# Performance work log

Hardware: AMD Instinct MI355X
Metric: run time of the kernel (lower is better)

Reference implementation:

```python
import jax, jax.numpy as jnp
import numpy as np

D = 512    # feature_dim
NH = 8     # n_head
LQ = 1024  # query length
LK = 1024  # key/value length
B = 4      # batch
TEMP = 30.0


def setup_inputs() -> dict:
    key = jax.random.key(0)
    ks = jax.random.split(key, 10)
    s = (2.0 / D) ** 0.5  # init: normal(0, sqrt(2/out_features))
    t = lambda k, shp: jax.random.normal(k, shp, dtype=jnp.float32)
    return {
        'query_real': t(ks[0], (LQ, B, D)),
        'query_imag': t(ks[1], (LQ, B, D)),
        'key_real': t(ks[2], (LK, B, D)),
        'key_imag': t(ks[3], (LK, B, D)),
        'value_real': t(ks[4], (LK, B, D)),
        'value_imag': t(ks[5], (LK, B, D)),
        # per-head stacked Linear weights [NH, out, in] (torch Linear: x @ W.T + b)
        'WK_real': t(ks[6], (NH, D, D)) * s,
        'WK_imag': t(ks[7], (NH, D, D)) * s,
        'WV_real': t(ks[8], (NH, D, D)) * s,
        'WV_imag': t(ks[9], (NH, D, D)) * s,
        'bK_real': jnp.zeros((NH, D), jnp.float32),
        'bK_imag': jnp.zeros((NH, D), jnp.float32),
        'bV_real': jnp.zeros((NH, D), jnp.float32),
        'bV_imag': jnp.zeros((NH, D), jnp.float32),
    }


def reference(query_real, query_imag, key_real, key_imag, value_real, value_imag,
              WK_real, WK_imag, WV_real, WV_imag,
              bK_real, bK_imag, bV_real, bV_imag):
    # stacked per-head linear: x [L,B,D], W [H,E,D], b [H,E] -> [H,L,B,E]
    lin = lambda x, W, b: jnp.einsum('lbd,hed->hlbe', x, W) + b[:, None, None, :]
    # complex projection of keys with WK (real/imag parts)
    kr = lin(key_real, WK_real, bK_real) - lin(key_imag, WK_imag, bK_imag)
    ki = lin(key_real, WK_imag, bK_imag) + lin(key_imag, WK_real, bK_real)
    # queries are projected with the WV weights (as in the source)
    qr = lin(query_real, WV_real, bV_real) - lin(query_imag, WV_imag, bV_imag)
    qi = lin(query_real, WV_imag, bV_imag) + lin(query_imag, WV_real, bV_real)
    # complex dot product q*k (no conjugate), magnitude -> scores [H,B,Lq,Lk]
    dr = jnp.einsum('hqbd,hpbd->hbqp', qr, kr) - jnp.einsum('hqbd,hpbd->hbqp', qi, ki)
    di = jnp.einsum('hqbd,hpbd->hbqp', qi, kr) + jnp.einsum('hqbd,hpbd->hbqp', qr, ki)
    mag = jnp.sqrt(dr * dr + di * di)
    aff = jax.nn.softmax(mag * TEMP, axis=-1)  # softmax over keys
    # weighted value sum; values are the RAW inputs (not projected)
    out_real = jnp.einsum('hbqp,pbd->qbhd', aff, value_real).reshape(LQ, B, NH * D)
    out_imag = jnp.einsum('hbqp,pbd->qbhd', aff, value_imag).reshape(LQ, B, NH * D)
    return out_real, out_imag
```

## Files before the change

kernel.cpp:

```cpp
#include <hip/hip_runtime.h>
#include <math.h>

typedef _Float16 h8_t __attribute__((ext_vector_type(8)));
typedef _Float16 h4_t __attribute__((ext_vector_type(4)));
typedef float    f4_t __attribute__((ext_vector_type(4)));

#define MFMA16(a, b, c) __builtin_amdgcn_mfma_f32_16x16x32_f16((a), (b), (c), 0, 0, 0)

typedef const __attribute__((address_space(1))) void* gas1_t;
typedef __attribute__((address_space(3))) void* las3_t;
__device__ __forceinline__ void gload16(const void* g, void* l) {
  __builtin_amdgcn_global_load_lds((gas1_t)g, (las3_t)l, 16, 0, 0);
}

constexpr int L   = 1024;
constexpr int NB  = 4;
constexpr int NHh = 8;
constexpr int D   = 512;
constexpr int M1  = L * NB;
constexpr int K1  = 2 * D;
constexpr int N1  = NHh * 2 * D;
constexpr int HB  = NHh * NB;

constexpr size_t PL_A2 = (size_t)HB * L * K1 * 2;
constexpr size_t PL_BS = (size_t)HB * 3 * L * D * 2;
constexpr size_t OFF_R0 = 0;
constexpr size_t OFF_A2 = 134217728;
constexpr size_t OFF_BS = OFF_A2 + 2 * PL_A2;
constexpr size_t OFF_VT = OFF_BS + 2 * PL_BS;
constexpr size_t WS_NEED = OFF_VT + (size_t)NB * 1024 * 1024 * 2;
constexpr size_t PL_AX = (size_t)M1 * K1 * 2;
constexpr size_t ST_AQ = 0;
constexpr size_t ST_AK = 2 * PL_AX;
constexpr size_t PL_W  = (size_t)N1 * K1 * 2;
constexpr size_t ST_WQ = 4 * PL_AX;
constexpr size_t ST_WK = ST_WQ + 2 * PL_W;

static __device__ __forceinline__ void split32(float x, _Float16& hi, _Float16& lo) {
  _Float16 h = (_Float16)x;
  hi = h;
  lo = (_Float16)(x - (float)h);
}


__global__ void k_stage_x(const float* __restrict__ qre, const float* __restrict__ qim,
                          const float* __restrict__ kre, const float* __restrict__ kim,
                          _Float16* __restrict__ qhi, _Float16* __restrict__ qlo,
                          _Float16* __restrict__ khi, _Float16* __restrict__ klo) {
  const float* re; const float* im; _Float16* hi; _Float16* lo;
  if (blockIdx.y == 0) { re = qre; im = qim; hi = qhi; lo = qlo; }
  else                 { re = kre; im = kim; hi = khi; lo = klo; }
  int t = blockIdx.x * 256 + threadIdx.x;
  size_t idx = (size_t)t * 4;
  int m = (int)(idx >> 10), k = (int)(idx & 1023);
  const float* src = (k < 512) ? (re + (size_t)m * 512 + k) : (im + (size_t)m * 512 + (k - 512));
  f4_t v = *reinterpret_cast<const f4_t*>(src);
  h4_t h, l;
#pragma unroll
  for (int j = 0; j < 4; ++j) {
    _Float16 hh, ll; split32(v[j], hh, ll); h[j] = hh; l[j] = ll;
  }
  int sw = ((m >> 1) & 3) << 3;
  size_t dst = (size_t)m * 1024 + (k ^ sw);
  *reinterpret_cast<h4_t*>(hi + dst) = h;
  *reinterpret_cast<h4_t*>(lo + dst) = l;
}

__global__ void k_stage_w(const float* __restrict__ WVr, const float* __restrict__ WVi,
                          const float* __restrict__ WKr, const float* __restrict__ WKi,
                          _Float16* __restrict__ qhi, _Float16* __restrict__ qlo,
                          _Float16* __restrict__ khi, _Float16* __restrict__ klo) {
  const float* Wr; const float* Wi; _Float16* hi; _Float16* lo;
  if (blockIdx.y == 0) { Wr = WVr; Wi = WVi; hi = qhi; lo = qlo; }
  else                 { Wr = WKr; Wi = WKi; hi = khi; lo = klo; }
  int t = blockIdx.x * 256 + threadIdx.x;
  size_t idx = (size_t)t * 4;
  int n = (int)(idx >> 10), k = (int)(idx & 1023);
  int h = n >> 10, ri = (n >> 9) & 1, e = n & 511;
  size_t rowoff = ((size_t)(h * 512 + e)) * 512;
  const float* src; float sgn = 1.0f;
  if (ri == 0) {
    if (k < 512) src = Wr + rowoff + k;
    else { src = Wi + rowoff + (k - 512); sgn = -1.0f; }
  } else {
    if (k < 512) src = Wi + rowoff + k;
    else src = Wr + rowoff + (k - 512);
  }
  f4_t v = *reinterpret_cast<const f4_t*>(src);
  h4_t h4, l4;
#pragma unroll
  for (int j = 0; j < 4; ++j) {
    _Float16 hh, ll; split32(sgn * v[j], hh, ll); h4[j] = hh; l4[j] = ll;
  }
  int sw = ((n >> 1) & 3) << 3;
  size_t dst = (size_t)n * 1024 + (k ^ sw);
  *reinterpret_cast<h4_t*>(hi + dst) = h4;
  *reinterpret_cast<h4_t*>(lo + dst) = l4;
}

__global__ void k_stage_v(const float* __restrict__ vr, const float* __restrict__ vi,
                          _Float16* __restrict__ vt) {
  __shared__ float tile[64][65];
  int pt = blockIdx.x, nt = blockIdx.y, b = blockIdx.z;
  const float* src = (nt < 8) ? vr : vi;
  int dbase = (nt & 7) * 64;
  for (int i = threadIdx.x; i < 4096; i += 256) {
    int pl = i >> 6, dl = i & 63;
    tile[pl][dl] = src[((size_t)(pt * 64 + pl) * 4 + b) * 512 + dbase + dl];
  }
  __syncthreads();
  for (int i = threadIdx.x; i < 4096; i += 256) {
    int nl = i >> 6, pl = i & 63;
    int psw = pl ^ ((nl & 7) << 3);
    vt[((size_t)b * 1024 + nt * 64 + nl) * 1024 + pt * 64 + psw] = (_Float16)tile[pl][nl];
  }
}

__global__ __launch_bounds__(512, 1) void k_proj(
    const _Float16* __restrict__ Ahi, const _Float16* __restrict__ Alo,
    const _Float16* __restrict__ Bhi, const _Float16* __restrict__ Blo,
    const float* __restrict__ biasR, const float* __restrict__ biasI,
    _Float16* __restrict__ OutHi, _Float16* __restrict__ OutLo, int mode) {
  extern __shared__ __align__(16) _Float16 dldsP[];
  const int tid = threadIdx.x;
  const int id = blockIdx.x;
  const int xcd = id & 7, j = id >> 3;
  const int cm = j >> 2, cn = j & 3;
  const int m0 = cm * 256;
  const int n0 = (xcd * 4 + cn) * 256;
  const int wid = tid >> 6, lane = tid & 63;
  const int wm = (wid >> 1) * 64, wn = (wid & 1) * 128;
  const int fr = lane & 15, fq = lane >> 4;
  const int csw = (fq ^ ((fr >> 1) & 3)) * 8;

  const int srow = tid >> 2, sslot = tid & 3;
  const int soff = srow * 32 + sslot * 8;
  const _Float16* gA0 = Ahi + (size_t)(m0 + srow) * 1024 + sslot * 8;
  const _Float16* gA1 = gA0 + 128 * 1024;
  const _Float16* gA2 = Alo + (size_t)(m0 + srow) * 1024 + sslot * 8;
  const _Float16* gA3 = gA2 + 128 * 1024;
  const _Float16* gB0 = Bhi + (size_t)(n0 + srow) * 1024 + sslot * 8;
  const _Float16* gB1 = gB0 + 128 * 1024;
  const _Float16* gB2 = Blo + (size_t)(n0 + srow) * 1024 + sslot * 8;
  const _Float16* gB3 = gB2 + 128 * 1024;

  auto STAGE = [&](int buf) {
    _Float16* Lb = dldsP + buf * 32768;
    gload16(gA0, &Lb[soff]);
    gload16(gA1, &Lb[4096 + soff]);
    gload16(gA2, &Lb[8192 + soff]);
    gload16(gA3, &Lb[12288 + soff]);
    gload16(gB0, &Lb[16384 + soff]);
    gload16(gB1, &Lb[20480 + soff]);
    gload16(gB2, &Lb[24576 + soff]);
    gload16(gB3, &Lb[28672 + soff]);
    gA0 += 32; gA1 += 32; gA2 += 32; gA3 += 32;
    gB0 += 32; gB1 += 32; gB2 += 32; gB3 += 32;
  };

  f4_t acc[4][8] = {};
  auto compute = [&](int buf) {
    const _Float16* Lb = dldsP + buf * 32768;
    h8_t af[4][2];
#pragma unroll
    for (int mi = 0; mi < 4; ++mi) {
      int r = wm + mi * 16 + fr;
      af[mi][0] = *reinterpret_cast<const h8_t*>(&Lb[r * 32 + csw]);
      af[mi][1] = *reinterpret_cast<const h8_t*>(&Lb[8192 + r * 32 + csw]);
    }
#pragma unroll
    for (int ni = 0; ni < 8; ++ni) {
      int rn = wn + ni * 16 + fr;
      h8_t bh = *reinterpret_cast<const h8_t*>(&Lb[16384 + rn * 32 + csw]);
      h8_t bl = *reinterpret_cast<const h8_t*>(&Lb[24576 + rn * 32 + csw]);
#pragma unroll
      for (int mi = 0; mi < 4; ++mi) {
        acc[mi][ni] = MFMA16(af[mi][0], bh, acc[mi][ni]);
        acc[mi][ni] = MFMA16(af[mi][0], bl, acc[mi][ni]);
        acc[mi][ni] = MFMA16(af[mi][1], bh, acc[mi][ni]);
      }
    }
  };

  STAGE(0);
  for (int kt = 0; kt < 31; ++kt) {
    __builtin_amdgcn_s_barrier();
    STAGE((kt + 1) & 1);
    asm volatile("s_waitcnt vmcnt(8)" ::: "memory");
    __builtin_amdgcn_s_barrier();
    compute(kt & 1);
  }
  __builtin_amdgcn_s_barrier();
  asm volatile("s_waitcnt vmcnt(0)" ::: "memory");
  __builtin_amdgcn_s_barrier();
  compute(1);

#pragma unroll
  for (int mi = 0; mi < 4; ++mi)
#pragma unroll
    for (int ni = 0; ni < 8; ++ni)
#pragma unroll
      for (int r = 0; r < 4; ++r) {
        int m = m0 + wm + mi * 16 + fq * 4 + r;
        int n = n0 + wn + ni * 16 + fr;
        int h = n >> 10, ri = (n >> 9) & 1, e = n & 511;
        float bias = (ri == 0) ? (biasR[h * 512 + e] - biasI[h * 512 + e])
                               : (biasI[h * 512 + e] + biasR[h * 512 + e]);
        float val = acc[mi][ni][r] + bias;
        _Float16 hi, lo; split32(val, hi, lo);
        int lb = m & 3;
        int lrow = m >> 2;
        int hb = h * 4 + lb;
        int sw = ((lrow >> 1) & 3) << 3;
        if (mode == 0) {
          size_t dst = ((size_t)hb * 1024 + lrow) * 1024 + ((ri * 512 + e) ^ sw);
          OutHi[dst] = hi; OutLo[dst] = lo;
        } else {
          int esw = e ^ sw;
          if (ri == 0) {
            size_t dst = (((size_t)hb * 3 + 0) * 1024 + lrow) * 512 + esw;
            OutHi[dst] = hi; OutLo[dst] = lo;
          } else {
            size_t d1 = (((size_t)hb * 3 + 1) * 1024 + lrow) * 512 + esw;
            size_t d2 = (((size_t)hb * 3 + 2) * 1024 + lrow) * 512 + esw;
            OutHi[d1] = hi;  OutLo[d1] = lo;
            OutHi[d2] = -hi; OutLo[d2] = -lo;
          }
        }
      }
}

__global__ __launch_bounds__(512, 1) void k_score(
    const _Float16* __restrict__ A2hi, const _Float16* __restrict__ A2lo,
    const _Float16* __restrict__ BShi, const _Float16* __restrict__ BSlo,
    float* __restrict__ mag) {
  extern __shared__ __align__(16) _Float16 dldsS[];
  const int tid = threadIdx.x;
  const int id = blockIdx.x;
  const int xcd = id & 7, j = id >> 3;
  const int hb = xcd * 4 + (j >> 5);
  const int r5 = j & 31;
  const int m0 = (r5 >> 3) * 256, n0 = (r5 & 7) * 128;
  const int wid = tid >> 6, lane = tid & 63;
  const int wm = (wid >> 1) * 64, wn = (wid & 1) * 64;
  const int fr = lane & 15, fq = lane >> 4;
  const int csw = (fq ^ ((fr >> 1) & 3)) * 8;

  const _Float16* Abh = A2hi + (size_t)hb * 1048576;
  const _Float16* Abl = A2lo + (size_t)hb * 1048576;
  const _Float16* BShb = BShi + (size_t)hb * 3 * 524288;
  const _Float16* BSlb = BSlo + (size_t)hb * 3 * 524288;

  const int srow = tid >> 2, sslot = tid & 3;
  const int soff = srow * 32 + sslot * 8;
  const size_t bbase = (size_t)(n0 + srow) * 512 + sslot * 8;
  const _Float16* gA0 = Abh + (size_t)(m0 + srow) * 1024 + sslot * 8;
  const _Float16* gA1 = gA0 + 128 * 1024;
  const _Float16* gA2 = Abl + (size_t)(m0 + srow) * 1024 + sslot * 8;
  const _Float16* gA3 = gA2 + 128 * 1024;
  const _Float16* gB0 = BShb + bbase;
  const _Float16* gB1 = BSlb + bbase;
  const _Float16* gB2 = BShb + 524288 + bbase;
  const _Float16* gB3 = BSlb + 524288 + bbase;

  auto STAGE = [&](int buf, int kt) {
    if (kt == 16) {
      gB0 = BShb + 2 * 524288 + bbase;
      gB1 = BSlb + 2 * 524288 + bbase;
      gB2 = BShb + bbase;
      gB3 = BSlb + bbase;
    }
    _Float16* Lb = dldsS + buf * 32768;
    gload16(gA0, &Lb[soff]);
    gload16(gA1, &Lb[4096 + soff]);
    gload16(gA2, &Lb[8192 + soff]);
    gload16(gA3, &Lb[12288 + soff]);
    gload16(gB0, &Lb[16384 + soff]);
    gload16(gB1, &Lb[20480 + soff]);
    gload16(gB2, &Lb[24576 + soff]);
    gload16(gB3, &Lb[28672 + soff]);
    gA0 += 32; gA1 += 32; gA2 += 32; gA3 += 32;
    gB0 += 32; gB1 += 32; gB2 += 32; gB3 += 32;
  };

  f4_t adr[4][4] = {}, adi[4][4] = {};
  auto compute = [&](int buf) {
    const _Float16* Lb = dldsS + buf * 32768;
    h8_t af[4][2];
#pragma unroll
    for (int mi = 0; mi < 4; ++mi) {
      int r = wm + mi * 16 + fr;
      af[mi][0] = *reinterpret_cast<const h8_t*>(&Lb[r * 32 + csw]);
      af[mi][1] = *reinterpret_cast<const h8_t*>(&Lb[8192 + r * 32 + csw]);
    }
#pragma unroll
    for (int ni = 0; ni < 4; ++ni) {
      int rn = wn + ni * 16 + fr;
      h8_t drh = *reinterpret_cast<const h8_t*>(&Lb[16384 + rn * 32 + csw]);
      h8_t drl = *reinterpret_cast<const h8_t*>(&Lb[20480 + rn * 32 + csw]);
      h8_t dih = *reinterpret_cast<const h8_t*>(&Lb[24576 + rn * 32 + csw]);
      h8_t dil = *reinterpret_cast<const h8_t*>(&Lb[28672 + rn * 32 + csw]);
#pragma unroll
      for (int mi = 0; mi < 4; ++mi) {
        adr[mi][ni] = MFMA16(af[mi][0], drh, adr[mi][ni]);
        adr[mi][ni] = MFMA16(af[mi][0], drl, adr[mi][ni]);
        adr[mi][ni] = MFMA16(af[mi][1], drh, adr[mi][ni]);
        adi[mi][ni] = MFMA16(af[mi][0], dih, adi[mi][ni]);
        adi[mi][ni] = MFMA16(af[mi][0], dil, adi[mi][ni]);
        adi[mi][ni] = MFMA16(af[mi][1], dih, adi[mi][ni]);
      }
    }
  };

  STAGE(0, 0);
  for (int kt = 0; kt < 31; ++kt) {
    __builtin_amdgcn_s_barrier();
    STAGE((kt + 1) & 1, kt + 1);
    asm volatile("s_waitcnt vmcnt(8)" ::: "memory");
    __builtin_amdgcn_s_barrier();
    compute(kt & 1);
  }
  __builtin_amdgcn_s_barrier();
  asm volatile("s_waitcnt vmcnt(0)" ::: "memory");
  __builtin_amdgcn_s_barrier();
  compute(1);

  float* mb = mag + (size_t)hb * 1048576;
#pragma unroll
  for (int mi = 0; mi < 4; ++mi)
#pragma unroll
    for (int ni = 0; ni < 4; ++ni)
#pragma unroll
      for (int r = 0; r < 4; ++r) {
        int q = m0 + wm + mi * 16 + fq * 4 + r;
        int p = n0 + wn + ni * 16 + fr;
        float dr = adr[mi][ni][r], di = adi[mi][ni][r];
        mb[(size_t)q * 1024 + p] = sqrtf(dr * dr + di * di) * 30.0f;
      }
}

__global__ void k_softmax(const float* __restrict__ mag, _Float16* __restrict__ aff) {
  const size_t base = (size_t)blockIdx.x * 1024;
  const int q = blockIdx.x & 1023;
  const int sw = (q & 7) << 3;
  const int tid = threadIdx.x;
  const int wid = tid >> 6, lane = tid & 63;
  float v[4];
#pragma unroll
  for (int j = 0; j < 4; ++j) v[j] = mag[base + tid + j * 256];
  float mx = fmaxf(fmaxf(v[0], v[1]), fmaxf(v[2], v[3]));
#pragma unroll
  for (int o = 32; o > 0; o >>= 1) mx = fmaxf(mx, __shfl_xor(mx, o));
  __shared__ float red[8];
  if (lane == 0) red[wid] = mx;
  __syncthreads();
  mx = fmaxf(fmaxf(red[0], red[1]), fmaxf(red[2], red[3]));
  float e[4]; float s = 0.0f;
#pragma unroll
  for (int j = 0; j < 4; ++j) { e[j] = __expf(v[j] - mx); s += e[j]; }
#pragma unroll
  for (int o = 32; o > 0; o >>= 1) s += __shfl_xor(s, o);
  if (lane == 0) red[4 + wid] = s;
  __syncthreads();
  s = red[4] + red[5] + red[6] + red[7];
  float inv = 1.0f / s;
#pragma unroll
  for (int j = 0; j < 4; ++j) aff[base + j * 256 + (tid ^ sw)] = (_Float16)(e[j] * inv);
}

__global__ __launch_bounds__(256, 2) void k_pv(
    const _Float16* __restrict__ aff, const _Float16* __restrict__ vt,
    float* __restrict__ out) {
  extern __shared__ __align__(16) _Float16 dldsV[];
  const int tid = threadIdx.x;
  const int id = blockIdx.x;
  const int xcd = id & 7, j = id >> 3;
  const int b = xcd >> 1;
  const int h = (xcd & 1) * 4 + (j >> 6);
  const int hb = h * 4 + b;
  const int r6 = j & 63;
  const int m0 = (r6 >> 3) * 128, n0 = (r6 & 7) * 128;
  const int wid = tid >> 6, lane = tid & 63;
  const int wm = (wid >> 1) * 64, wn = (wid & 1) * 64;
  const int fr = lane & 15, fq = lane >> 4;
  const int s7 = fr & 7;

  const _Float16* Ab = aff + (size_t)hb * 1048576;
  const _Float16* Bb = vt + (size_t)b * 1048576;

  const int srow = tid >> 3, sslot = tid & 7;
  const int soff = srow * 64 + sslot * 8;
  const _Float16* gA = Ab + (size_t)(m0 + srow) * 1024 + sslot * 8;
  const _Float16* gB = Bb + (size_t)(n0 + srow) * 1024 + sslot * 8;

  auto STAGE = [&](int buf) {
    _Float16* Lb = dldsV + buf * 16384;
    gload16(gA,             &Lb[soff]);
    gload16(gA + 32 * 1024, &Lb[2048 + soff]);
    gload16(gA + 64 * 1024, &Lb[4096 + soff]);
    gload16(gA + 96 * 1024, &Lb[6144 + soff]);
    gload16(gB,             &Lb[8192 + soff]);
    gload16(gB + 32 * 1024, &Lb[10240 + soff]);
    gload16(gB + 64 * 1024, &Lb[12288 + soff]);
    gload16(gB + 96 * 1024, &Lb[14336 + soff]);
    gA += 64; gB += 64;
  };

  f4_t acc[4][4] = {};
  auto compute = [&](int buf) {
    const _Float16* Lb = dldsV + buf * 16384;
#pragma unroll
    for (int k32 = 0; k32 < 2; ++k32) {
      const int csw = ((k32 * 4 + fq) ^ s7) * 8;
      h8_t af[4];
#pragma unroll
      for (int mi = 0; mi < 4; ++mi)
        af[mi] = *reinterpret_cast<const h8_t*>(&Lb[(wm + mi * 16 + fr) * 64 + csw]);
#pragma unroll
      for (int ni = 0; ni < 4; ++ni) {
        h8_t bf = *reinterpret_cast<const h8_t*>(&Lb[8192 + (wn + ni * 16 + fr) * 64 + csw]);
#pragma unroll
        for (int mi = 0; mi < 4; ++mi) acc[mi][ni] = MFMA16(af[mi], bf, acc[mi][ni]);
      }
    }
  };

  STAGE(0);
  for (int kt = 0; kt < 15; ++kt) {
    __builtin_amdgcn_s_barrier();
    STAGE((kt + 1) & 1);
    asm volatile("s_waitcnt vmcnt(8)" ::: "memory");
    __builtin_amdgcn_s_barrier();
    compute(kt & 1);
  }
  __builtin_amdgcn_s_barrier();
  asm volatile("s_waitcnt vmcnt(0)" ::: "memory");
  __builtin_amdgcn_s_barrier();
  compute(1);

#pragma unroll
  for (int mi = 0; mi < 4; ++mi)
#pragma unroll
    for (int ni = 0; ni < 4; ++ni)
#pragma unroll
      for (int r = 0; r < 4; ++r) {
        int q = m0 + wm + mi * 16 + fq * 4 + r;
        int n = n0 + wn + ni * 16 + fr;
        int d = n & 511;
        size_t o = (size_t)(n < 512 ? 0 : 16777216) + (((size_t)q * 4 + b) * 8 + h) * 512 + d;
        out[o] = acc[mi][ni][r];
      }
}

extern "C" void kernel_launch(void* const* d_in, const int* in_sizes, int n_in,
                              void* d_out, int out_size, void* d_ws, size_t ws_size,
                              hipStream_t stream) {
  (void)in_sizes; (void)n_in; (void)out_size;
  if (ws_size < WS_NEED) return;

  hipFuncSetAttribute((const void*)k_score, hipFuncAttributeMaxDynamicSharedMemorySize, 131072);
  hipFuncSetAttribute((const void*)k_proj,  hipFuncAttributeMaxDynamicSharedMemorySize, 131072);
  hipFuncSetAttribute((const void*)k_pv,    hipFuncAttributeMaxDynamicSharedMemorySize, 65536);

  const float* qre = (const float*)d_in[0];
  const float* qim = (const float*)d_in[1];
  const float* kre = (const float*)d_in[2];
  const float* kim = (const float*)d_in[3];
  const float* vre = (const float*)d_in[4];
  const float* vim = (const float*)d_in[5];
  const float* WKr = (const float*)d_in[6];
  const float* WKi = (const float*)d_in[7];
  const float* WVr = (const float*)d_in[8];
  const float* WVi = (const float*)d_in[9];
  const float* bKr = (const float*)d_in[10];
  const float* bKi = (const float*)d_in[11];
  const float* bVr = (const float*)d_in[12];
  const float* bVi = (const float*)d_in[13];

  char* ws = (char*)d_ws;
  _Float16* AqHi = (_Float16*)(ws + ST_AQ);
  _Float16* AqLo = (_Float16*)(ws + ST_AQ + PL_AX);
  _Float16* AkHi = (_Float16*)(ws + ST_AK);
  _Float16* AkLo = (_Float16*)(ws + ST_AK + PL_AX);
  _Float16* WqHi = (_Float16*)(ws + ST_WQ);
  _Float16* WqLo = (_Float16*)(ws + ST_WQ + PL_W);
  _Float16* WkHi = (_Float16*)(ws + ST_WK);
  _Float16* WkLo = (_Float16*)(ws + ST_WK + PL_W);
  _Float16* A2Hi = (_Float16*)(ws + OFF_A2);
  _Float16* A2Lo = (_Float16*)(ws + OFF_A2 + PL_A2);
  _Float16* BSHi = (_Float16*)(ws + OFF_BS);
  _Float16* BSLo = (_Float16*)(ws + OFF_BS + PL_BS);
  _Float16* Vt   = (_Float16*)(ws + OFF_VT);
  float*    magp = (float*)(ws + OFF_R0);
  _Float16* affp = (_Float16*)(ws + OFF_A2);
  float*    outp = (float*)d_out;

  k_stage_x<<<dim3(4096, 2), dim3(256), 0, stream>>>(qre, qim, kre, kim, AqHi, AqLo, AkHi, AkLo);
  k_stage_w<<<dim3(8192, 2), dim3(256), 0, stream>>>(WVr, WVi, WKr, WKi, WqHi, WqLo, WkHi, WkLo);
  k_stage_v<<<dim3(16, 16, 4), dim3(256), 0, stream>>>(vre, vim, Vt);
  k_proj<<<dim3(512), dim3(512), 131072, stream>>>(AqHi, AqLo, WqHi, WqLo, bVr, bVi, A2Hi, A2Lo, 0);
  k_proj<<<dim3(512), dim3(512), 131072, stream>>>(AkHi, AkLo, WkHi, WkLo, bKr, bKi, BSHi, BSLo, 1);
  k_score<<<dim3(1024), dim3(512), 131072, stream>>>(A2Hi, A2Lo, BSHi, BSLo, magp);
  k_softmax<<<dim3(32 * 1024), dim3(256), 0, stream>>>(magp, affp);
  k_pv<<<dim3(2048), dim3(256), 65536, stream>>>(affp, Vt, outp);
}
```

Before: 937.6 us.

## Interleave split A/B global-to-LDS prefetch with halved MFMA phases and setprio

Restructures the main K-loop of both the projection GEMM and the score GEMM. Each iteration is split into two compute phases over half the N tiles, and the next-tile A and B global-to-LDS loads are issued separately between phases, separated by barriers. MFMA phases are wrapped in s_setprio(1) so memory issue and math from different waves interleave more finely. The cost is extra barriers per iteration and a full vmcnt(0) wait at the end of each iteration, which could expose load latency.

```diff
diff --git a/kernel.cpp b/kernel.cpp
--- a/kernel.cpp
+++ b/kernel.cpp
@@ -144,23 +144,32 @@
   const _Float16* gB2 = Blo + (size_t)(n0 + srow) * 1024 + sslot * 8;
   const _Float16* gB3 = gB2 + 128 * 1024;
 
-  auto STAGE = [&](int buf) {
+  auto STAGE_A = [&](int buf) {
     _Float16* Lb = dldsP + buf * 32768;
     gload16(gA0, &Lb[soff]);
     gload16(gA1, &Lb[4096 + soff]);
     gload16(gA2, &Lb[8192 + soff]);
     gload16(gA3, &Lb[12288 + soff]);
+    gA0 += 32; gA1 += 32; gA2 += 32; gA3 += 32;
+  };
+  auto STAGE_B = [&](int buf) {
+    _Float16* Lb = dldsP + buf * 32768;
     gload16(gB0, &Lb[16384 + soff]);
     gload16(gB1, &Lb[20480 + soff]);
     gload16(gB2, &Lb[24576 + soff]);
     gload16(gB3, &Lb[28672 + soff]);
-    gA0 += 32; gA1 += 32; gA2 += 32; gA3 += 32;
     gB0 += 32; gB1 += 32; gB2 += 32; gB3 += 32;
   };
 
   f4_t acc[4][8] = {};
-  auto compute = [&](int buf) {
-    const _Float16* Lb = dldsP + buf * 32768;
+
+  STAGE_A(0); STAGE_B(0);
+  asm volatile("s_waitcnt vmcnt(0)" ::: "memory");
+  __builtin_amdgcn_s_barrier();
+
+  for (int kt = 0; kt < 32; ++kt) {
+    const int cur = kt & 1, nxt = cur ^ 1;
+    const _Float16* Lb = dldsP + cur * 32768;
     h8_t af[4][2];
 #pragma unroll
     for (int mi = 0; mi < 4; ++mi) {
@@ -168,32 +177,47 @@
       af[mi][0] = *reinterpret_cast<const h8_t*>(&Lb[r * 32 + csw]);
       af[mi][1] = *reinterpret_cast<const h8_t*>(&Lb[8192 + r * 32 + csw]);
     }
-#pragma unroll
-    for (int ni = 0; ni < 8; ++ni) {
+    h8_t bh[4], bl[4];
+#pragma unroll
+    for (int ni = 0; ni < 4; ++ni) {
       int rn = wn + ni * 16 + fr;
-      h8_t bh = *reinterpret_cast<const h8_t*>(&Lb[16384 + rn * 32 + csw]);
-      h8_t bl = *reinterpret_cast<const h8_t*>(&Lb[24576 + rn * 32 + csw]);
+      bh[ni] = *reinterpret_cast<const h8_t*>(&Lb[16384 + rn * 32 + csw]);
+      bl[ni] = *reinterpret_cast<const h8_t*>(&Lb[24576 + rn * 32 + csw]);
+    }
+    if (kt < 31) STAGE_A(nxt);
+    __builtin_amdgcn_s_barrier();
+    __builtin_amdgcn_s_setprio(1);
+#pragma unroll
+    for (int ni = 0; ni < 4; ++ni)
 #pragma unroll
       for (int mi = 0; mi < 4; ++mi) {
-        acc[mi][ni] = MFMA16(af[mi][0], bh, acc[mi][ni]);
-        acc[mi][ni] = MFMA16(af[mi][0], bl, acc[mi][ni]);
-        acc[mi][ni] = MFMA16(af[mi][1], bh, acc[mi][ni]);
-      }
-    }
-  };
-
-  STAGE(0);
-  for (int kt = 0; kt < 31; ++kt) {
-    __builtin_amdgcn_s_barrier();
-    STAGE((kt + 1) & 1);
-    asm volatile("s_waitcnt vmcnt(8)" ::: "memory");
-    __builtin_amdgcn_s_barrier();
-    compute(kt & 1);
-  }
-  __builtin_amdgcn_s_barrier();
-  asm volatile("s_waitcnt vmcnt(0)" ::: "memory");
-  __builtin_amdgcn_s_barrier();
-  compute(1);
+        acc[mi][ni] = MFMA16(af[mi][0], bh[ni], acc[mi][ni]);
+        acc[mi][ni] = MFMA16(af[mi][0], bl[ni], acc[mi][ni]);
+        acc[mi][ni] = MFMA16(af[mi][1], bh[ni], acc[mi][ni]);
+      }
+    __builtin_amdgcn_s_setprio(0);
+    __builtin_amdgcn_s_barrier();
+#pragma unroll
+    for (int ni = 0; ni < 4; ++ni) {
+      int rn = wn + (ni + 4) * 16 + fr;
+      bh[ni] = *reinterpret_cast<const h8_t*>(&Lb[16384 + rn * 32 + csw]);
+      bl[ni] = *reinterpret_cast<const h8_t*>(&Lb[24576 + rn * 32 + csw]);
+    }
+    if (kt < 31) STAGE_B(nxt);
+    __builtin_amdgcn_s_barrier();
+    __builtin_amdgcn_s_setprio(1);
+#pragma unroll
+    for (int ni = 0; ni < 4; ++ni)
+#pragma unroll
+      for (int mi = 0; mi < 4; ++mi) {
+        acc[mi][ni + 4] = MFMA16(af[mi][0], bh[ni], acc[mi][ni + 4]);
+        acc[mi][ni + 4] = MFMA16(af[mi][0], bl[ni], acc[mi][ni + 4]);
+        acc[mi][ni + 4] = MFMA16(af[mi][1], bh[ni], acc[mi][ni + 4]);
+      }
+    __builtin_amdgcn_s_setprio(0);
+    if (kt < 31) asm volatile("s_waitcnt vmcnt(0)" ::: "memory");
+    __builtin_amdgcn_s_barrier();
+  }
 
 #pragma unroll
   for (int mi = 0; mi < 4; ++mi)
@@ -263,7 +287,15 @@
   const _Float16* gB2 = BShb + 524288 + bbase;
   const _Float16* gB3 = BSlb + 524288 + bbase;
 
-  auto STAGE = [&](int buf, int kt) {
+  auto STAGE_A = [&](int buf) {
+    _Float16* Lb = dldsS + buf * 32768;
+    gload16(gA0, &Lb[soff]);
+    gload16(gA1, &Lb[4096 + soff]);
+    gload16(gA2, &Lb[8192 + soff]);
+    gload16(gA3, &Lb[12288 + soff]);
+    gA0 += 32; gA1 += 32; gA2 += 32; gA3 += 32;
+  };
+  auto STAGE_B = [&](int buf, int kt) {
     if (kt == 16) {
       gB0 = BShb + 2 * 524288 + bbase;
       gB1 = BSlb + 2 * 524288 + bbase;
@@ -271,21 +303,22 @@
       gB3 = BSlb + bbase;
     }
     _Float16* Lb = dldsS + buf * 32768;
-    gload16(gA0, &Lb[soff]);
-    gload16(gA1, &Lb[4096 + soff]);
-    gload16(gA2, &Lb[8192 + soff]);
-    gload16(gA3, &Lb[12288 + soff]);
     gload16(gB0, &Lb[16384 + soff]);
     gload16(gB1, &Lb[20480 + soff]);
     gload16(gB2, &Lb[24576 + soff]);
     gload16(gB3, &Lb[28672 + soff]);
-    gA0 += 32; gA1 += 32; gA2 += 32; gA3 += 32;
     gB0 += 32; gB1 += 32; gB2 += 32; gB3 += 32;
   };
 
   f4_t adr[4][4] = {}, adi[4][4] = {};
-  auto compute = [&](int buf) {
-    const _Float16* Lb = dldsS + buf * 32768;
+
+  STAGE_A(0); STAGE_B(0, 0);
+  asm volatile("s_waitcnt vmcnt(0)" ::: "memory");
+  __builtin_amdgcn_s_barrier();
+
+  for (int kt = 0; kt < 32; ++kt) {
+    const int cur = kt & 1, nxt = cur ^ 1;
+    const _Float16* Lb = dldsS + cur * 32768;
     h8_t af[4][2];
 #pragma unroll
     for (int mi = 0; mi < 4; ++mi) {
@@ -293,37 +326,57 @@
       af[mi][0] = *reinterpret_cast<const h8_t*>(&Lb[r * 32 + csw]);
       af[mi][1] = *reinterpret_cast<const h8_t*>(&Lb[8192 + r * 32 + csw]);
     }
-#pragma unroll
-    for (int ni = 0; ni < 4; ++ni) {
+    h8_t drh[2], drl[2], dih[2], dil[2];
+#pragma unroll
+    for (int ni = 0; ni < 2; ++ni) {
       int rn = wn + ni * 16 + fr;
-      h8_t drh = *reinterpret_cast<const h8_t*>(&Lb[16384 + rn * 32 + csw]);
-      h8_t drl = *reinterpret_cast<const h8_t*>(&Lb[20480 + rn * 32 + csw]);
-      h8_t dih = *reinterpret_cast<const h8_t*>(&Lb[24576 + rn * 32 + csw]);
-      h8_t dil = *reinterpret_cast<const h8_t*>(&Lb[28672 + rn * 32 + csw]);
+      drh[ni] = *reinterpret_cast<const h8_t*>(&Lb[16384 + rn * 32 + csw]);
+      drl[ni] = *reinterpret_cast<const h8_t*>(&Lb[20480 + rn * 32 + csw]);
+      dih[ni] = *reinterpret_cast<const h8_t*>(&Lb[24576 + rn * 32 + csw]);
+      dil[ni] = *reinterpret_cast<const h8_t*>(&Lb[28672 + rn * 32 + csw]);
+    }
+    if (kt < 31) STAGE_A(nxt);
+    __builtin_amdgcn_s_barrier();
+    __builtin_amdgcn_s_setprio(1);
+#pragma unroll
+    for (int ni = 0; ni < 2; ++ni)
 #pragma unroll
       for (int mi = 0; mi < 4; ++mi) {
-        adr[mi][ni] = MFMA16(af[mi][0], drh, adr[mi][ni]);
-        adr[mi][ni] = MFMA16(af[mi][0], drl, adr[mi][ni]);
-        adr[mi][ni] = MFMA16(af[mi][1], drh, adr[mi][ni]);
-        adi[mi][ni] = MFMA16(af[mi][0], dih, adi[mi][ni]);
-        adi[mi][ni] = MFMA16(af[mi][0], dil, adi[mi][ni]);
-        adi[mi][ni] = MFMA16(af[mi][1], dih, adi[mi][ni]);
-      }
-    }
-  };
-
-  STAGE(0, 0);
-  for (int kt = 0; kt < 31; ++kt) {
-    __builtin_amdgcn_s_barrier();
-    STAGE((kt + 1) & 1, kt + 1);
-    asm volatile("s_waitcnt vmcnt(8)" ::: "memory");
-    __builtin_amdgcn_s_barrier();
-    compute(kt & 1);
-  }
-  __builtin_amdgcn_s_barrier();
-  asm volatile("s_waitcnt vmcnt(0)" ::: "memory");
-  __builtin_amdgcn_s_barrier();
-  compute(1);
+        adr[mi][ni] = MFMA16(af[mi][0], drh[ni], adr[mi][ni]);
+        adr[mi][ni] = MFMA16(af[mi][0], drl[ni], adr[mi][ni]);
+        adr[mi][ni] = MFMA16(af[mi][1], drh[ni], adr[mi][ni]);
+        adi[mi][ni] = MFMA16(af[mi][0], dih[ni], adi[mi][ni]);
+        adi[mi][ni] = MFMA16(af[mi][0], dil[ni], adi[mi][ni]);
+        adi[mi][ni] = MFMA16(af[mi][1], dih[ni], adi[mi][ni]);
+      }
+    __builtin_amdgcn_s_setprio(0);
+    __builtin_amdgcn_s_barrier();
+#pragma unroll
+    for (int ni = 0; ni < 2; ++ni) {
+      int rn = wn + (ni + 2) * 16 + fr;
+      drh[ni] = *reinterpret_cast<const h8_t*>(&Lb[16384 + rn * 32 + csw]);
+      drl[ni] = *reinterpret_cast<const h8_t*>(&Lb[20480 + rn * 32 + csw]);
+      dih[ni] = *reinterpret_cast<const h8_t*>(&Lb[24576 + rn * 32 + csw]);
+      dil[ni] = *reinterpret_cast<const h8_t*>(&Lb[28672 + rn * 32 + csw]);
+    }
+    if (kt < 31) STAGE_B(nxt, kt + 1);
+    __builtin_amdgcn_s_barrier();
+    __builtin_amdgcn_s_setprio(1);
+#pragma unroll
+    for (int ni = 0; ni < 2; ++ni)
+#pragma unroll
+      for (int mi = 0; mi < 4; ++mi) {
+        adr[mi][ni + 2] = MFMA16(af[mi][0], drh[ni], adr[mi][ni + 2]);
+        adr[mi][ni + 2] = MFMA16(af[mi][0], drl[ni], adr[mi][ni + 2]);
+        adr[mi][ni + 2] = MFMA16(af[mi][1], drh[ni], adr[mi][ni + 2]);
+        adi[mi][ni + 2] = MFMA16(af[mi][0], dih[ni], adi[mi][ni + 2]);
+        adi[mi][ni + 2] = MFMA16(af[mi][0], dil[ni], adi[mi][ni + 2]);
+        adi[mi][ni + 2] = MFMA16(af[mi][1], dih[ni], adi[mi][ni + 2]);
+      }
+    __builtin_amdgcn_s_setprio(0);
+    if (kt < 31) asm volatile("s_waitcnt vmcnt(0)" ::: "memory");
+    __builtin_amdgcn_s_barrier();
+  }
 
   float* mb = mag + (size_t)hb * 1048576;
 #pragma unroll
```

After: 907.8 us. 1.03x faster.

## Interleave LDS reads, global prefetch and MFMA phases with barriers and setprio

Applied to the files above, without the earlier changes.

Both the projection and score GEMM main loops are restructured into four phases per K-tile. Each phase reads a slice of B fragments from LDS and issues half of the next tile's global-to-LDS loads, then runs MFMAs at raised wave priority. This aims to overlap memory traffic with matrix math and keep waves in lockstep, ping-pong style. It adds many more barriers per iteration and a full vmcnt(0) wait before the last phase, which may stall if loads are slow.

```diff
diff --git a/kernel.cpp b/kernel.cpp
--- a/kernel.cpp
+++ b/kernel.cpp
@@ -144,56 +144,90 @@
   const _Float16* gB2 = Blo + (size_t)(n0 + srow) * 1024 + sslot * 8;
   const _Float16* gB3 = gB2 + 128 * 1024;
 
-  auto STAGE = [&](int buf) {
+  auto STAGE_A = [&](int buf) {
     _Float16* Lb = dldsP + buf * 32768;
     gload16(gA0, &Lb[soff]);
     gload16(gA1, &Lb[4096 + soff]);
     gload16(gA2, &Lb[8192 + soff]);
     gload16(gA3, &Lb[12288 + soff]);
+    gA0 += 32; gA1 += 32; gA2 += 32; gA3 += 32;
+  };
+  auto STAGE_B = [&](int buf) {
+    _Float16* Lb = dldsP + buf * 32768;
     gload16(gB0, &Lb[16384 + soff]);
     gload16(gB1, &Lb[20480 + soff]);
     gload16(gB2, &Lb[24576 + soff]);
     gload16(gB3, &Lb[28672 + soff]);
-    gA0 += 32; gA1 += 32; gA2 += 32; gA3 += 32;
     gB0 += 32; gB1 += 32; gB2 += 32; gB3 += 32;
   };
 
   f4_t acc[4][8] = {};
-  auto compute = [&](int buf) {
-    const _Float16* Lb = dldsP + buf * 32768;
-    h8_t af[4][2];
-#pragma unroll
-    for (int mi = 0; mi < 4; ++mi) {
-      int r = wm + mi * 16 + fr;
-      af[mi][0] = *reinterpret_cast<const h8_t*>(&Lb[r * 32 + csw]);
-      af[mi][1] = *reinterpret_cast<const h8_t*>(&Lb[8192 + r * 32 + csw]);
-    }
-#pragma unroll
-    for (int ni = 0; ni < 8; ++ni) {
-      int rn = wn + ni * 16 + fr;
-      h8_t bh = *reinterpret_cast<const h8_t*>(&Lb[16384 + rn * 32 + csw]);
-      h8_t bl = *reinterpret_cast<const h8_t*>(&Lb[24576 + rn * 32 + csw]);
-#pragma unroll
-      for (int mi = 0; mi < 4; ++mi) {
-        acc[mi][ni] = MFMA16(af[mi][0], bh, acc[mi][ni]);
-        acc[mi][ni] = MFMA16(af[mi][0], bl, acc[mi][ni]);
-        acc[mi][ni] = MFMA16(af[mi][1], bh, acc[mi][ni]);
-      }
-    }
-  };
-
-  STAGE(0);
-  for (int kt = 0; kt < 31; ++kt) {
-    __builtin_amdgcn_s_barrier();
-    STAGE((kt + 1) & 1);
-    asm volatile("s_waitcnt vmcnt(8)" ::: "memory");
-    __builtin_amdgcn_s_barrier();
-    compute(kt & 1);
-  }
-  __builtin_amdgcn_s_barrier();
+  h8_t af[4][2];
+  h8_t bh0, bl0, bh1, bl1;
+
+#define PROJ_READ_AF()                                                       \
+  _Pragma("unroll")                                                          \
+  for (int mi = 0; mi < 4; ++mi) {                                           \
+    int r = wm + mi * 16 + fr;                                               \
+    af[mi][0] = *reinterpret_cast<const h8_t*>(&LB[r * 32 + csw]);           \
+    af[mi][1] = *reinterpret_cast<const h8_t*>(&LB[8192 + r * 32 + csw]);    \
+  }
+
+#define PROJ_READ_B(P)                                                       \
+  { int rn0 = wn + (2 * (P)) * 16 + fr;                                      \
+    int rn1 = wn + (2 * (P) + 1) * 16 + fr;                                  \
+    bh0 = *reinterpret_cast<const h8_t*>(&LB[16384 + rn0 * 32 + csw]);       \
+    bl0 = *reinterpret_cast<const h8_t*>(&LB[24576 + rn0 * 32 + csw]);       \
+    bh1 = *reinterpret_cast<const h8_t*>(&LB[16384 + rn1 * 32 + csw]);       \
+    bl1 = *reinterpret_cast<const h8_t*>(&LB[24576 + rn1 * 32 + csw]); }
+
+#define PROJ_MFMA(P)                                                         \
+  _Pragma("unroll")                                                          \
+  for (int mi = 0; mi < 4; ++mi) {                                           \
+    acc[mi][2 * (P)]     = MFMA16(af[mi][0], bh0, acc[mi][2 * (P)]);         \
+    acc[mi][2 * (P)]     = MFMA16(af[mi][0], bl0, acc[mi][2 * (P)]);         \
+    acc[mi][2 * (P)]     = MFMA16(af[mi][1], bh0, acc[mi][2 * (P)]);         \
+    acc[mi][2 * (P) + 1] = MFMA16(af[mi][0], bh1, acc[mi][2 * (P) + 1]);     \
+    acc[mi][2 * (P) + 1] = MFMA16(af[mi][0], bl1, acc[mi][2 * (P) + 1]);     \
+    acc[mi][2 * (P) + 1] = MFMA16(af[mi][1], bh1, acc[mi][2 * (P) + 1]);     \
+  }
+
+  STAGE_A(0); STAGE_B(0);
   asm volatile("s_waitcnt vmcnt(0)" ::: "memory");
   __builtin_amdgcn_s_barrier();
-  compute(1);
+
+  for (int kt = 0; kt < 32; ++kt) {
+    const int cur = kt & 1, nxt = cur ^ 1;
+    const _Float16* LB = dldsP + cur * 32768;
+    PROJ_READ_AF();
+    PROJ_READ_B(0);
+    if (kt < 31) STAGE_A(nxt);
+    __builtin_amdgcn_s_barrier();
+    __builtin_amdgcn_s_setprio(1);
+    PROJ_MFMA(0);
+    __builtin_amdgcn_s_setprio(0);
+    __builtin_amdgcn_s_barrier();
+    PROJ_READ_B(1);
+    if (kt < 31) STAGE_B(nxt);
+    __builtin_amdgcn_s_barrier();
+    __builtin_amdgcn_s_setprio(1);
+    PROJ_MFMA(1);
+    __builtin_amdgcn_s_setprio(0);
+    __builtin_amdgcn_s_barrier();
+    PROJ_READ_B(2);
+    __builtin_amdgcn_s_barrier();
+    __builtin_amdgcn_s_setprio(1);
+    PROJ_MFMA(2);
+    __builtin_amdgcn_s_setprio(0);
+    __builtin_amdgcn_s_barrier();
+    PROJ_READ_B(3);
+    asm volatile("s_waitcnt vmcnt(0)" ::: "memory");
+    __builtin_amdgcn_s_barrier();
+    __builtin_amdgcn_s_setprio(1);
+    PROJ_MFMA(3);
+    __builtin_amdgcn_s_setprio(0);
+    __builtin_amdgcn_s_barrier();
+  }
 
 #pragma unroll
   for (int mi = 0; mi < 4; ++mi)
@@ -263,67 +297,95 @@
   const _Float16* gB2 = BShb + 524288 + bbase;
   const _Float16* gB3 = BSlb + 524288 + bbase;
 
-  auto STAGE = [&](int buf, int kt) {
-    if (kt == 16) {
+  auto STAGE_A = [&](int buf) {
+    _Float16* Lb = dldsS + buf * 32768;
+    gload16(gA0, &Lb[soff]);
+    gload16(gA1, &Lb[4096 + soff]);
+    gload16(gA2, &Lb[8192 + soff]);
+    gload16(gA3, &Lb[12288 + soff]);
+    gA0 += 32; gA1 += 32; gA2 += 32; gA3 += 32;
+  };
+  auto STAGE_B = [&](int buf, int ktn) {
+    if (ktn == 16) {
       gB0 = BShb + 2 * 524288 + bbase;
       gB1 = BSlb + 2 * 524288 + bbase;
       gB2 = BShb + bbase;
       gB3 = BSlb + bbase;
     }
     _Float16* Lb = dldsS + buf * 32768;
-    gload16(gA0, &Lb[soff]);
-    gload16(gA1, &Lb[4096 + soff]);
-    gload16(gA2, &Lb[8192 + soff]);
-    gload16(gA3, &Lb[12288 + soff]);
     gload16(gB0, &Lb[16384 + soff]);
     gload16(gB1, &Lb[20480 + soff]);
     gload16(gB2, &Lb[24576 + soff]);
     gload16(gB3, &Lb[28672 + soff]);
-    gA0 += 32; gA1 += 32; gA2 += 32; gA3 += 32;
     gB0 += 32; gB1 += 32; gB2 += 32; gB3 += 32;
   };
 
   f4_t adr[4][4] = {}, adi[4][4] = {};
-  auto compute = [&](int buf) {
-    const _Float16* Lb = dldsS + buf * 32768;
-    h8_t af[4][2];
-#pragma unroll
-    for (int mi = 0; mi < 4; ++mi) {
-      int r = wm + mi * 16 + fr;
-      af[mi][0] = *reinterpret_cast<const h8_t*>(&Lb[r * 32 + csw]);
-      af[mi][1] = *reinterpret_cast<const h8_t*>(&Lb[8192 + r * 32 + csw]);
-    }
-#pragma unroll
-    for (int ni = 0; ni < 4; ++ni) {
-      int rn = wn + ni * 16 + fr;
-      h8_t drh = *reinterpret_cast<const h8_t*>(&Lb[16384 + rn * 32 + csw]);
-      h8_t drl = *reinterpret_cast<const h8_t*>(&Lb[20480 + rn * 32 + csw]);
-      h8_t dih = *reinterpret_cast<const h8_t*>(&Lb[24576 + rn * 32 + csw]);
-      h8_t dil = *reinterpret_cast<const h8_t*>(&Lb[28672 + rn * 32 + csw]);
-#pragma unroll
-      for (int mi = 0; mi < 4; ++mi) {
-        adr[mi][ni] = MFMA16(af[mi][0], drh, adr[mi][ni]);
-        adr[mi][ni] = MFMA16(af[mi][0], drl, adr[mi][ni]);
-        adr[mi][ni] = MFMA16(af[mi][1], drh, adr[mi][ni]);
-        adi[mi][ni] = MFMA16(af[mi][0], dih, adi[mi][ni]);
-        adi[mi][ni] = MFMA16(af[mi][0], dil, adi[mi][ni]);
-        adi[mi][ni] = MFMA16(af[mi][1], dih, adi[mi][ni]);
-      }
-    }
-  };
-
-  STAGE(0, 0);
-  for (int kt = 0; kt < 31; ++kt) {
-    __builtin_amdgcn_s_barrier();
-    STAGE((kt + 1) & 1, kt + 1);
-    asm volatile("s_waitcnt vmcnt(8)" ::: "memory");
-    __builtin_amdgcn_s_barrier();
-    compute(kt & 1);
-  }
-  __builtin_amdgcn_s_barrier();
+  h8_t af[4][2];
+  h8_t bdh, bdl, bih, bil;
+
+#define SCORE_READ_AF()                                                      \
+  _Pragma("unroll")                                                          \
+  for (int mi = 0; mi < 4; ++mi) {                                           \
+    int r = wm + mi * 16 + fr;                                               \
+    af[mi][0] = *reinterpret_cast<const h8_t*>(&LB[r * 32 + csw]);           \
+    af[mi][1] = *reinterpret_cast<const h8_t*>(&LB[8192 + r * 32 + csw]);    \
+  }
+
+#define SCORE_READ_B(NI)                                                     \
+  { int rn = wn + (NI) * 16 + fr;                                            \
+    bdh = *reinterpret_cast<const h8_t*>(&LB[16384 + rn * 32 + csw]);        \
+    bdl = *reinterpret_cast<const h8_t*>(&LB[20480 + rn * 32 + csw]);        \
+    bih = *reinterpret_cast<const h8_t*>(&LB[24576 + rn * 32 + csw]);        \
+    bil = *reinterpret_cast<const h8_t*>(&LB[28672 + rn * 32 + csw]); }
+
+#define SCORE_MFMA(NI)                                                       \
+  _Pragma("unroll")                                                          \
+  for (int mi = 0; mi < 4; ++mi) {                                           \
+    adr[mi][NI] = MFMA16(af[mi][0], bdh, adr[mi][NI]);                       \
+    adr[mi][NI] = MFMA16(af[mi][0], bdl, adr[mi][NI]);                       \
+    adr[mi][NI] = MFMA16(af[mi][1], bdh, adr[mi][NI]);                       \
+    adi[mi][NI] = MFMA16(af[mi][0], bih, adi[mi][NI]);                       \
+    adi[mi][NI] = MFMA16(af[mi][0], bil, adi[mi][NI]);                       \
+    adi[mi][NI] = MFMA16(af[mi][1], bih, adi[mi][NI]);                       \
+  }
+
+  STAGE_A(0); STAGE_B(0, 0);
   asm volatile("s_waitcnt vmcnt(0)" ::: "memory");
   __builtin_amdgcn_s_barrier();
-  compute(1);
+
+  for (int kt = 0; kt < 32; ++kt) {
+    const int cur = kt & 1, nxt = cur ^ 1;
+    const _Float16* LB = dldsS + cur * 32768;
+    SCORE_READ_AF();
+    SCORE_READ_B(0);
+    if (kt < 31) STAGE_A(nxt);
+    __builtin_amdgcn_s_barrier();
+    __builtin_amdgcn_s_setprio(1);
+    SCORE_MFMA(0);
+    __builtin_amdgcn_s_setprio(0);
+    __builtin_amdgcn_s_barrier();
+    SCORE_READ_B(1);
+    if (kt < 31) STAGE_B(nxt, kt + 1);
+    __builtin_amdgcn_s_barrier();
+    __builtin_amdgcn_s_setprio(1);
+    SCORE_MFMA(1);
+    __builtin_amdgcn_s_setprio(0);
+    __builtin_amdgcn_s_barrier();
+    SCORE_READ_B(2);
+    __builtin_amdgcn_s_barrier();
+    __builtin_amdgcn_s_setprio(1);
+    SCORE_MFMA(2);
+    __builtin_amdgcn_s_setprio(0);
+    __builtin_amdgcn_s_barrier();
+    SCORE_READ_B(3);
+    asm volatile("s_waitcnt vmcnt(0)" ::: "memory");
+    __builtin_amdgcn_s_barrier();
+    __builtin_amdgcn_s_setprio(1);
+    SCORE_MFMA(3);
+    __builtin_amdgcn_s_setprio(0);
+    __builtin_amdgcn_s_barrier();
+  }
 
   float* mb = mag + (size_t)hb * 1048576;
 #pragma unroll
```

Result: no change. 923.2 us (-1.5%).
